# Kernel optimization log

Hardware: AMD Instinct MI355X
Metric: run time of the kernel (lower is better)

Reference implementation:

```python
import jax, jax.numpy as jnp
import numpy as np

# Mamba-2 config (from MambaBackbone defaults)
D_MODEL = 512
D_STATE = 64
D_CONV = 4
EXPAND = 2
HEADDIM = 64
CHUNK = 256
D_INNER = EXPAND * D_MODEL            # 1024
NHEADS = D_INNER // HEADDIM           # 16
CONV_DIM = D_INNER + 2 * D_STATE      # 1152 (ngroups=1)
D_IN_PROJ = 2 * D_INNER + 2 * D_STATE + NHEADS  # 2192


def setup_inputs() -> dict:
    key = jax.random.key(0)
    ks = jax.random.split(key, 8)
    B, T = 4, 4096
    x = jax.random.normal(ks[0], (B, T, D_MODEL), dtype=jnp.float32)
    W_in = jax.random.normal(ks[1], (D_IN_PROJ, D_MODEL), dtype=jnp.float32) * 0.02
    conv_w = jax.random.normal(ks[2], (CONV_DIM, D_CONV), dtype=jnp.float32) * 0.2
    conv_b = jnp.zeros((CONV_DIM,), jnp.float32)
    # dt_bias initialized so softplus(dt_bias) ~ Uniform-log[1e-3, 1e-1] (mamba2 init)
    dt0 = jnp.exp(jax.random.uniform(ks[3], (NHEADS,)) * (np.log(0.1) - np.log(0.001)) + np.log(0.001))
    dt_bias = dt0 + jnp.log(-jnp.expm1(-dt0))
    A_log = jnp.log(jnp.arange(1, NHEADS + 1, dtype=jnp.float32))  # A = -exp(A_log) in [-16,-1]
    D = jnp.ones((NHEADS,), jnp.float32)
    norm_w = jnp.ones((D_INNER,), jnp.float32)
    W_out = jax.random.normal(ks[4], (D_MODEL, D_INNER), dtype=jnp.float32) * 0.02
    return dict(x=x, W_in=W_in, conv_w=conv_w, conv_b=conv_b, dt_bias=dt_bias,
                A_log=A_log, D=D, norm_w=norm_w, W_out=W_out)


def segsum(a):
    """a: (..., l) -> (..., l, l) with [i,j] = sum_{j<k<=i} a[..,k]; -inf above diag."""
    l = a.shape[-1]
    cs = jnp.cumsum(a, axis=-1)
    ss = cs[..., :, None] - cs[..., None, :]
    mask = jnp.tril(jnp.ones((l, l), dtype=bool))
    return jnp.where(mask, ss, -jnp.inf)


def reference(x, W_in, conv_w, conv_b, dt_bias, A_log, D, norm_w, W_out):
    Bb, T, _ = x.shape
    # input projection -> [z | xBC | dt]
    zxbcdt = x @ W_in.T                                    # (B,T,2192)
    z = zxbcdt[..., :D_INNER]
    xBC = zxbcdt[..., D_INNER:D_INNER + CONV_DIM]
    dt = zxbcdt[..., -NHEADS:]
    # causal depthwise conv1d (kernel D_CONV) + SiLU
    xp = jnp.pad(xBC, ((0, 0), (D_CONV - 1, 0), (0, 0)))
    conv = sum(xp[:, k:k + T, :] * conv_w[:, k] for k in range(D_CONV)) + conv_b
    xBC = jax.nn.silu(conv)
    xs = xBC[..., :D_INNER].reshape(Bb, T, NHEADS, HEADDIM)  # (B,T,H,P)
    Bm = xBC[..., D_INNER:D_INNER + D_STATE]                 # (B,T,N)  ngroups=1
    Cm = xBC[..., D_INNER + D_STATE:]                        # (B,T,N)
    dt = jax.nn.softplus(dt + dt_bias)                       # (B,T,H)
    A = -jnp.exp(A_log)                                      # (H,)
    # ---- chunked SSD (Mamba-2) ----
    nc = T // CHUNK
    Ad = (dt * A).reshape(Bb, nc, CHUNK, NHEADS).transpose(0, 3, 1, 2)   # (b,h,c,l) log-decay
    x_dt = (xs * dt[..., None]).reshape(Bb, nc, CHUNK, NHEADS, HEADDIM)  # (b,c,l,h,p)
    Bc = Bm.reshape(Bb, nc, CHUNK, D_STATE)                              # (b,c,l,n)
    Cc = Cm.reshape(Bb, nc, CHUNK, D_STATE)
    A_cs = jnp.cumsum(Ad, axis=-1)                                       # (b,h,c,l)
    L = jnp.exp(segsum(Ad))                                              # (b,h,c,l,l)
    # intra-chunk (diagonal blocks)
    Y_diag = jnp.einsum('bcln,bcsn,bhcls,bcshp->bclhp', Cc, Bc, L, x_dt)
    # per-chunk end states
    decay_states = jnp.exp(A_cs[..., -1:] - A_cs)                        # (b,h,c,l)
    states = jnp.einsum('bcln,bhcl,bclhp->cbhpn', Bc, decay_states, x_dt)
    chunk_decay = jnp.exp(A_cs[..., -1]).transpose(2, 0, 1)              # (c,b,h)
    def step(h, inp):
        dec, st = inp
        return dec[..., None, None] * h + st, h                          # emit state BEFORE chunk
    h0 = jnp.zeros_like(states[0])
    _, prev = jax.lax.scan(step, h0, (chunk_decay, states))              # (c,b,h,p,n)
    # inter-chunk contribution
    Y_off = jnp.einsum('bcln,cbhpn,bhcl->bclhp', Cc, prev, jnp.exp(A_cs))
    y = (Y_diag + Y_off).reshape(Bb, T, NHEADS, HEADDIM) + D[None, None, :, None] * xs
    y = y.reshape(Bb, T, D_INNER)
    # gated RMSNorm: rmsnorm(y * silu(z)) * w   (norm_before_gate=False)
    yz = y * jax.nn.silu(z)
    out = yz * jax.lax.rsqrt(jnp.mean(yz * yz, axis=-1, keepdims=True) + 1e-5) * norm_w
    return out @ W_out.T
```

## Files before the change

### kernel.cpp

```cpp
#include <hip/hip_runtime.h>
#include <hip/hip_bf16.h>
#include <cstdint>

typedef unsigned int  uint;
typedef unsigned short ushort;
using bf16 = __hip_bfloat16;

#define B_     4
#define T_     4096
#define DM     512
#define DI     1024
#define DSTATE 64
#define HD     64
#define NH     16
#define NC     16
#define CHK    256
#define CONVD  1152
#define DPROJ  2192

using f32x4 = __attribute__((ext_vector_type(4))) float;
using s16x8 = __attribute__((ext_vector_type(8))) short;

#define MFMA16(a, b, c) __builtin_amdgcn_mfma_f32_16x16x32_bf16((a), (b), (c), 0, 0, 0)

__device__ inline void unpack8(const uint4 v, float* f) {
  const uint w[4] = {v.x, v.y, v.z, v.w};
#pragma unroll
  for (int i = 0; i < 4; ++i) {
    f[2*i]   = __uint_as_float(w[i] << 16);
    f[2*i+1] = __uint_as_float(w[i] & 0xffff0000u);
  }
}
__device__ inline void unpack4(const uint2 v, float* f) {
  f[0] = __uint_as_float(v.x << 16); f[1] = __uint_as_float(v.x & 0xffff0000u);
  f[2] = __uint_as_float(v.y << 16); f[3] = __uint_as_float(v.y & 0xffff0000u);
}
__device__ inline ushort bfbits(float a) {
  bf16 h = __float2bfloat16(a);
  return *reinterpret_cast<ushort*>(&h);
}
__device__ inline uint pack2(float a, float b) {
  return (uint)bfbits(a) | ((uint)bfbits(b) << 16);
}
__device__ inline uint4 pack8(const float* f) {
  uint4 v;
  v.x = pack2(f[0], f[1]); v.y = pack2(f[2], f[3]);
  v.z = pack2(f[4], f[5]); v.w = pack2(f[6], f[7]);
  return v;
}

__device__ __forceinline__ void gl_lds16(const void* g, void* l) {
  __builtin_amdgcn_global_load_lds(
      (const __attribute__((address_space(1))) unsigned int*)g,
      (__attribute__((address_space(3))) unsigned int*)l, 16, 0, 0);
}

__global__ __launch_bounds__(256)
void cast_bf16(const float* __restrict__ in, short* __restrict__ out, int n8) {
  const int i = blockIdx.x * 256 + threadIdx.x;
  if (i >= n8) return;
  float f[8];
  float4 a = *reinterpret_cast<const float4*>(&in[(size_t)i * 8]);
  float4 b = *reinterpret_cast<const float4*>(&in[(size_t)i * 8 + 4]);
  f[0]=a.x; f[1]=a.y; f[2]=a.z; f[3]=a.w; f[4]=b.x; f[5]=b.y; f[6]=b.z; f[7]=b.w;
  *reinterpret_cast<uint4*>(&out[(size_t)i * 8]) = pack8(f);
}

template<int EPI>
__global__ __launch_bounds__(256)
void gemm_mfma(const short* __restrict__ A, const short* __restrict__ Bw,
               int K, int N, int nbx, float* __restrict__ Cout,
               short* __restrict__ z, short* __restrict__ xbc,
               float* __restrict__ dtp, const float* __restrict__ dt_bias) {
  __shared__ __align__(16) char smem[(EPI == 1) ? 34816 : 32768];
  short* As = reinterpret_cast<short*>(smem);
  short* Bs = As + 128 * 64;
  const int tid  = threadIdx.x;
  const int lane = tid & 63, w = tid >> 6;
  const int hi = lane >> 4, lo = lane & 15;
  const int lx = lo & 7;
  const int wr = w >> 1, wc = w & 1;

  const int cpx = gridDim.x >> 3;
  const int swz = (blockIdx.x & 7) * cpx + (blockIdx.x >> 3);
  const int bm = (swz / nbx) * 128, bn = (swz % nbx) * 128;

  f32x4 acc[4][4] = {};

  const int srow = lane >> 3;
  const int scol = ((lane & 7) ^ srow) * 8;

  for (int k0 = 0; k0 < K; k0 += 64) {
#pragma unroll
    for (int i = 0; i < 4; ++i) {
      const int seg = w * 4 + i;
      const int row = seg * 8 + srow;
      gl_lds16(&A[(size_t)(bm + row) * K + k0 + scol], &As[seg * 512]);
      const int brow = (bn + row < N) ? (bn + row) : (N - 1);
      gl_lds16(&Bw[(size_t)brow * K + k0 + scol], &Bs[seg * 512]);
    }
    __syncthreads();
#pragma unroll
    for (int kb = 0; kb < 2; ++kb) {
      s16x8 af[4], bf[4];
#pragma unroll
      for (int t = 0; t < 4; ++t) {
        const int gg = ((kb * 4 + hi) ^ lx) * 8;
        af[t] = *reinterpret_cast<const s16x8*>(&As[(wr*64 + t*16 + lo) * 64 + gg]);
        bf[t] = *reinterpret_cast<const s16x8*>(&Bs[(wc*64 + t*16 + lo) * 64 + gg]);
      }
#pragma unroll
      for (int lt = 0; lt < 4; ++lt)
#pragma unroll
        for (int nt = 0; nt < 4; ++nt)
          acc[lt][nt] = MFMA16(af[lt], bf[nt], acc[lt][nt]);
    }
    __syncthreads();
  }

  if (EPI == 0) {
#pragma unroll
    for (int lt = 0; lt < 4; ++lt)
#pragma unroll
      for (int nt = 0; nt < 4; ++nt) {
        const int cg = bn + wc * 64 + nt * 16 + lo;
#pragma unroll
        for (int r = 0; r < 4; ++r) {
          const int rg = bm + wr * 64 + lt * 16 + hi * 4 + r;
          Cout[(size_t)rg * DM + cg] = acc[lt][nt][r];
        }
      }
  } else {
    if (bn + 128 > DI + CONVD) {
#pragma unroll
      for (int lt = 0; lt < 4; ++lt)
#pragma unroll
        for (int nt = 0; nt < 4; ++nt) {
          const int cg = bn + wc * 64 + nt * 16 + lo;
          if (cg >= DI + CONVD && cg < DPROJ) {
            const float bia = dt_bias[cg - DI - CONVD];
#pragma unroll
            for (int r = 0; r < 4; ++r) {
              const int rg = bm + wr * 64 + lt * 16 + hi * 4 + r;
              const float v = acc[lt][nt][r] + bia;
              dtp[(size_t)rg * NH + (cg - DI - CONVD)] =
                  (v > 20.f) ? v : log1pf(expf(v));
            }
          }
        }
    }
    ushort (*tile)[136] = reinterpret_cast<ushort(*)[136]>(smem);
    __syncthreads();
#pragma unroll
    for (int lt = 0; lt < 4; ++lt)
#pragma unroll
      for (int nt = 0; nt < 4; ++nt) {
        const int cl = wc * 64 + nt * 16 + lo;
#pragma unroll
        for (int r = 0; r < 4; ++r)
          tile[wr * 64 + lt * 16 + hi * 4 + r][cl] = bfbits(acc[lt][nt][r]);
      }
    __syncthreads();
#pragma unroll
    for (int it = 0; it < 8; ++it) {
      const int unit = it * 256 + tid;
      const int row = unit >> 4;
      const int c8  = (unit & 15) << 3;
      const int cg  = bn + c8;
      const int rg  = bm + row;
      if (cg >= DI + CONVD) continue;
      uint4 v = *reinterpret_cast<const uint4*>(&tile[row][c8]);
      if (cg < DI)
        *reinterpret_cast<uint4*>(&reinterpret_cast<ushort*>(z)[(size_t)rg * DI + cg]) = v;
      else
        *reinterpret_cast<uint4*>(&reinterpret_cast<ushort*>(xbc)[(size_t)rg * CONVD + (cg - DI)]) = v;
    }
  }
}

__global__ __launch_bounds__(256)
void conv_silu(const short* __restrict__ xbc, const float* __restrict__ cw,
               const float* __restrict__ cb, short* __restrict__ xc) {
  const int idx = blockIdx.x * 256 + threadIdx.x;
  const int cp = idx % 288;
  const int tb = idx / 288;
  const int ch = cp * 4;
  const int b  = tb >> 9;
  const int t0 = (tb & 511) << 3;
  const long base = ((long)b * T_ + t0) * CONVD + ch;

  float4 wv[4];
#pragma unroll
  for (int c = 0; c < 4; ++c)
    wv[c] = *reinterpret_cast<const float4*>(&cw[(ch + c) * 4]);
  const float4 bi = *reinterpret_cast<const float4*>(&cb[ch]);
  const float bias[4] = {bi.x, bi.y, bi.z, bi.w};

  float v[11][4];
#pragma unroll
  for (int i = 0; i < 11; ++i) {
    const int t = t0 - 3 + i;
    if (t >= 0) {
      const uint2 u = *reinterpret_cast<const uint2*>(&xbc[base + (long)(i - 3) * CONVD]);
      unpack4(u, v[i]);
    } else { v[i][0] = v[i][1] = v[i][2] = v[i][3] = 0.f; }
  }
#pragma unroll
  for (int j = 0; j < 8; ++j) {
    float s[4];
#pragma unroll
    for (int c = 0; c < 4; ++c) {
      s[c] = bias[c] + v[j][c]*wv[c].x + v[j+1][c]*wv[c].y
           + v[j+2][c]*wv[c].z + v[j+3][c]*wv[c].w;
      s[c] = s[c] / (1.f + __expf(-s[c]));
    }
    uint2 o; o.x = pack2(s[0], s[1]); o.y = pack2(s[2], s[3]);
    *reinterpret_cast<uint2*>(&xc[base + (long)j * CONVD]) = o;
  }
}

__global__ __launch_bounds__(256)
void ssd_states(const short* __restrict__ xc, const float* __restrict__ dtp,
                const float* __restrict__ A_log,
                float* __restrict__ acs_g, float* __restrict__ states) {
  const int bid = blockIdx.x;
  const int h = bid >> 6, b = (bid >> 4) & 3, c = bid & 15;
  const int tid = threadIdx.x;
  const int lane = tid & 63, w = tid >> 6;
  const int hi = lane >> 4, lo = lane & 15;

  __shared__ __align__(16) float acs[CHK];
  __shared__ float wsum[4];
  __shared__ __align__(16) uint Btm2[64 * 36];
  __shared__ __align__(16) uint Xdm2[64 * 36];

  const size_t row0 = (size_t)b * T_ + (size_t)c * CHK;

  const float Ah = -expf(A_log[h]);
  float v = dtp[(row0 + tid) * NH + h] * Ah;
#pragma unroll
  for (int off = 1; off < 64; off <<= 1) {
    const float u = __shfl_up(v, off);
    if (lane >= off) v += u;
  }
  if (lane == 63) wsum[w] = v;
  __syncthreads();
  float pre = 0.f;
#pragma unroll
  for (int ww = 0; ww < 4; ++ww) if (ww < w) pre += wsum[ww];
  v += pre;
  acs[tid] = v;
  acs_g[(((size_t)b * NH + h) * NC + c) * CHK + tid] = v;
  __syncthreads();
  const float acs_last = acs[CHK - 1];

  f32x4 stacc[4] = {};
  const int sp2 = tid & 31;
  const int g   = tid >> 5;

  for (int ss = 0; ss < 4; ++ss) {
    const int s0 = ss * 64;
    {
      const int se = s0 + 2 * sp2;
      const size_t re = (row0 + se) * (size_t)CONVD;
      const size_t ro = re + CONVD;
      uint4 bqe = *reinterpret_cast<const uint4*>(&xc[re + DI + g*8]);
      uint4 bqo = *reinterpret_cast<const uint4*>(&xc[ro + DI + g*8]);
      uint4 xqe = *reinterpret_cast<const uint4*>(&xc[re + h*HD + g*8]);
      uint4 xqo = *reinterpret_cast<const uint4*>(&xc[ro + h*HD + g*8]);
      const float de_ = dtp[(row0 + se) * NH + h] * __expf(acs_last - acs[se]);
      const float do_ = dtp[(row0 + se + 1) * NH + h] * __expf(acs_last - acs[se + 1]);
      const ushort* beu = reinterpret_cast<const ushort*>(&bqe);
      const ushort* bou = reinterpret_cast<const ushort*>(&bqo);
      float fe[8], fo[8];
      unpack8(xqe, fe); unpack8(xqo, fo);
#pragma unroll
      for (int j = 0; j < 8; ++j) {
        const int cidx = (g * 8 + j) * 36 + sp2;
        Btm2[cidx] = (uint)beu[j] | ((uint)bou[j] << 16);
        Xdm2[cidx] = pack2(fe[j] * de_, fo[j] * do_);
      }
    }
    __syncthreads();
#pragma unroll
    for (int kb = 0; kb < 2; ++kb) {
      s16x8 xdf = *reinterpret_cast<const s16x8*>(&Xdm2[(w*16 + lo)*36 + kb*16 + hi*4]);
#pragma unroll
      for (int nt = 0; nt < 4; ++nt) {
        s16x8 btf = *reinterpret_cast<const s16x8*>(&Btm2[(nt*16 + lo)*36 + kb*16 + hi*4]);
        stacc[nt] = MFMA16(xdf, btf, stacc[nt]);
      }
    }
    __syncthreads();
  }

  const size_t sbase = (((size_t)c * B_ + b) * NH + h) * (HD * DSTATE);
#pragma unroll
  for (int nt = 0; nt < 4; ++nt) {
    const int n = nt*16 + lo;
#pragma unroll
    for (int r = 0; r < 4; ++r) {
      const int p = w*16 + hi*4 + r;
      states[sbase + (size_t)p * DSTATE + n] = stacc[nt][r];
    }
  }
}

__global__ __launch_bounds__(256)
void chunk_scan(const float* __restrict__ acs_g, const float* __restrict__ st,
                short* __restrict__ pv) {
  const int idx = blockIdx.x * 256 + threadIdx.x;
  const int pn = idx & 4095;
  const int h  = (idx >> 12) & 15;
  const int b  = idx >> 16;
  float hst = 0.f;
#pragma unroll
  for (int c = 0; c < NC; ++c) {
    const size_t o = (((size_t)c * B_ + b) * NH + h) * 4096 + pn;
    reinterpret_cast<ushort*>(pv)[o] = bfbits(hst);
    const float dec = __expf(acs_g[(((size_t)b * NH + h) * NC + c) * CHK + CHK - 1]);
    hst = dec * hst + st[o];
  }
}

__global__ __launch_bounds__(256, 2)
void ssd_y(const short* __restrict__ xc, const float* __restrict__ dtp,
           const float* __restrict__ acs_g, const short* __restrict__ pv,
           const float* __restrict__ Dvec, short* __restrict__ y) {
  const int bid = blockIdx.x;
  const int h = bid >> 6, b = (bid >> 4) & 3, c = bid & 15;
  const int tid = threadIdx.x;
  const int lane = tid & 63, w = tid >> 6;
  const int hi = lane >> 4, lo = lane & 15;

  __shared__ __align__(16) float acs[CHK];
  __shared__ __align__(16) float ds[CHK];
  __shared__ __align__(16) short Bsm[64 * 64];
  __shared__ __align__(16) uint Xtm2[64 * 36];
  __shared__ __align__(16) short Pb[4][16][72];

  const size_t row0 = (size_t)b * T_ + (size_t)c * CHK;
  const float* acg = &acs_g[(((size_t)b * NH + h) * NC + c) * CHK];

  acs[tid] = acg[tid];
  __syncthreads();
  ds[tid] = (tid > 0) ? __expf(acs[tid] - acs[tid - 1]) : 1.f;

  s16x8 creg[4][2];
#pragma unroll
  for (int lt = 0; lt < 4; ++lt)
#pragma unroll
    for (int kb = 0; kb < 2; ++kb)
      creg[lt][kb] = *reinterpret_cast<const s16x8*>(
          &xc[(row0 + w*64 + lt*16 + lo) * CONVD + DI + DSTATE + kb*32 + hi*8]);

  f32x4 yacc[4][4] = {};
  {
    const short* pvb = &pv[(((size_t)c * B_ + b) * NH + h) * 4096];
    __builtin_amdgcn_s_setprio(1);
#pragma unroll
    for (int kb = 0; kb < 2; ++kb) {
      s16x8 pf[4];
#pragma unroll
      for (int pt = 0; pt < 4; ++pt)
        pf[pt] = *reinterpret_cast<const s16x8*>(&pvb[(pt*16 + lo) * DSTATE + kb*32 + hi*8]);
#pragma unroll
      for (int pt = 0; pt < 4; ++pt)
#pragma unroll
        for (int lt = 0; lt < 4; ++lt)
          yacc[pt][lt] = MFMA16(pf[pt], creg[lt][kb], yacc[pt][lt]);
    }
    __builtin_amdgcn_s_setprio(0);
  }
  __syncthreads();
#pragma unroll
  for (int lt = 0; lt < 4; ++lt) {
    const float el = __expf(acs[w*64 + lt*16 + lo]);
#pragma unroll
    for (int pt = 0; pt < 4; ++pt)
#pragma unroll
      for (int r = 0; r < 4; ++r) yacc[pt][lt][r] *= el;
  }

  const int sp2 = tid & 31;
  const int g   = tid >> 5;
  const int srow8 = lane >> 3;
  const int gsrc  = ((lane & 7) ^ srow8) * 8;

  for (int ss = 0; ss < 4; ++ss) {
    const int s0 = ss * 64;
#pragma unroll
    for (int i = 0; i < 2; ++i) {
      const int seg = w * 2 + i;
      gl_lds16(&xc[(row0 + s0 + seg * 8 + srow8) * (size_t)CONVD + DI + gsrc],
               &Bsm[seg * 512]);
    }
    {
      const int se = s0 + 2 * sp2;
      const size_t re = (row0 + se) * (size_t)CONVD;
      uint4 xqe = *reinterpret_cast<const uint4*>(&xc[re + h*HD + g*8]);
      uint4 xqo = *reinterpret_cast<const uint4*>(&xc[re + CONVD + h*HD + g*8]);
      const float de_ = dtp[(row0 + se) * NH + h];
      const float do_ = dtp[(row0 + se + 1) * NH + h];
      float fe[8], fo[8];
      unpack8(xqe, fe); unpack8(xqo, fo);
#pragma unroll
      for (int j = 0; j < 8; ++j)
        Xtm2[(g * 8 + j) * 36 + sp2] = pack2(fe[j] * de_, fo[j] * do_);
    }
    __syncthreads();

    if (ss <= w) {
#pragma unroll
      for (int lt = 0; lt < 4; ++lt) {
        f32x4 sacc[4] = {};
        __builtin_amdgcn_s_setprio(1);
#pragma unroll
        for (int st = 0; st < 4; ++st) {
          const int r = st * 16 + lo;
          s16x8 b0 = *reinterpret_cast<const s16x8*>(&Bsm[r*64 + ((0*4 + hi) ^ (lo & 7)) * 8]);
          s16x8 b1 = *reinterpret_cast<const s16x8*>(&Bsm[r*64 + ((1*4 + hi) ^ (lo & 7)) * 8]);
          sacc[st] = MFMA16(b0, creg[lt][0], sacc[st]);
          sacc[st] = MFMA16(b1, creg[lt][1], sacc[st]);
        }
        __builtin_amdgcn_s_setprio(0);
        const int lg = w*64 + lt*16 + lo;
        const float al = acs[lg];
#pragma unroll
        for (int st = 0; st < 4; ++st) {
          const int sb = s0 + st*16 + hi*4;
          float wv[4];
          wv[3] = __expf(al - acs[sb + 3]);
          wv[2] = wv[3] * ds[sb + 3];
          wv[1] = wv[2] * ds[sb + 2];
          wv[0] = wv[1] * ds[sb + 1];
          float p4[4];
#pragma unroll
          for (int r = 0; r < 4; ++r)
            p4[r] = (sb + r <= lg) ? sacc[st][r] * wv[r] : 0.f;
          uint2 pk; pk.x = pack2(p4[0], p4[1]); pk.y = pack2(p4[2], p4[3]);
          *reinterpret_cast<uint2*>(&Pb[w][lo][st*16 + hi*4]) = pk;
        }
        __builtin_amdgcn_s_setprio(1);
#pragma unroll
        for (int kb = 0; kb < 2; ++kb) {
          s16x8 pfr = *reinterpret_cast<const s16x8*>(&Pb[w][lo][kb*32 + hi*8]);
#pragma unroll
          for (int pt = 0; pt < 4; ++pt) {
            s16x8 xfr = *reinterpret_cast<const s16x8*>(&Xtm2[(pt*16 + lo)*36 + kb*16 + hi*4]);
            yacc[pt][lt] = MFMA16(xfr, pfr, yacc[pt][lt]);
          }
        }
        __builtin_amdgcn_s_setprio(0);
      }
    }
    __syncthreads();
  }

  const float Dh = Dvec[h];
#pragma unroll
  for (int lt = 0; lt < 4; ++lt) {
    const int l = w*64 + lt*16 + lo;
    ushort* yrow = reinterpret_cast<ushort*>(&y[(row0 + l) * DI + h * HD]);
    const short* xrow = &xc[(row0 + l) * CONVD + h * HD];
#pragma unroll
    for (int pt = 0; pt < 4; ++pt) {
      const int p0 = pt*16 + hi*4;
      uint2 xb2 = *reinterpret_cast<const uint2*>(&xrow[p0]);
      float xf[4]; unpack4(xb2, xf);
      float o[4];
#pragma unroll
      for (int r = 0; r < 4; ++r) o[r] = yacc[pt][lt][r] + Dh * xf[r];
      uint2 pk; pk.x = pack2(o[0], o[1]); pk.y = pack2(o[2], o[3]);
      *reinterpret_cast<uint2*>(&yrow[p0]) = pk;
    }
  }
}

__global__ __launch_bounds__(256)
void gate_rmsnorm(const short* __restrict__ z, const float* __restrict__ norm_w,
                  short* __restrict__ y) {
  const int row = blockIdx.x;
  const int tid = threadIdx.x;
  const short* zrow = &z[(size_t)row * DI];
  short* yrow = &y[(size_t)row * DI];
  uint2 yb = *reinterpret_cast<const uint2*>(&yrow[tid * 4]);
  uint2 zb = *reinterpret_cast<const uint2*>(&zrow[tid * 4]);
  float yv[4], zv[4];
  unpack4(yb, yv); unpack4(zb, zv);
  float tq[4];
  float ss = 0.f;
#pragma unroll
  for (int j = 0; j < 4; ++j) {
    const float sil = zv[j] / (1.f + __expf(-zv[j]));
    tq[j] = yv[j] * sil;
    ss += tq[j] * tq[j];
  }
#pragma unroll
  for (int off = 32; off >= 1; off >>= 1) ss += __shfl_down(ss, off);
  __shared__ float red[4];
  if ((tid & 63) == 0) red[tid >> 6] = ss;
  __syncthreads();
  const float tot = red[0] + red[1] + red[2] + red[3];
  const float r = rsqrtf(tot * (1.f / (float)DI) + 1e-5f);
  float4 wv = *reinterpret_cast<const float4*>(&norm_w[tid * 4]);
  uint2 ob;
  ob.x = pack2(tq[0] * r * wv.x, tq[1] * r * wv.y);
  ob.y = pack2(tq[2] * r * wv.z, tq[3] * r * wv.w);
  *reinterpret_cast<uint2*>(&yrow[tid * 4]) = ob;
}

extern "C" void kernel_launch(void* const* d_in, const int* in_sizes, int n_in,
                              void* d_out, int out_size, void* d_ws, size_t ws_size,
                              hipStream_t stream) {
  const float* x       = (const float*)d_in[0];
  const float* W_in    = (const float*)d_in[1];
  const float* conv_w  = (const float*)d_in[2];
  const float* conv_b  = (const float*)d_in[3];
  const float* dt_bias = (const float*)d_in[4];
  const float* A_log   = (const float*)d_in[5];
  const float* Dv      = (const float*)d_in[6];
  const float* norm_w  = (const float*)d_in[7];
  const float* W_out   = (const float*)d_in[8];
  float* out = (float*)d_out;

  char* w0 = (char*)d_ws;
  short* z    = (short*)(w0);
  short* xbc  = (short*)(w0 + 33554432ULL);
  short* xc   = (short*)(w0 + 71303168ULL);
  short* wob  = (short*)(w0 + 109051904ULL);
  float* dtp  = (float*)(w0 + 111149056ULL);
  float* acs  = (float*)(w0 + 112197632ULL);
  float* st   = (float*)(w0 + 113246208ULL);
  short* pv   = (short*)(w0 + 130023424ULL);
  short* xb   = xc;
  short* wb   = (short*)st;
  short* y    = xbc;

  const int M = B_ * T_;

  cast_bf16<<<(M * DM / 8 + 255) / 256, 256, 0, stream>>>(x, xb, M * DM / 8);
  cast_bf16<<<(DPROJ * DM / 8 + 255) / 256, 256, 0, stream>>>(W_in, wb, DPROJ * DM / 8);
  cast_bf16<<<(DM * DI / 8 + 255) / 256, 256, 0, stream>>>(W_out, wob, DM * DI / 8);

  const int nbx_in = (DPROJ + 127) / 128;
  gemm_mfma<1><<<nbx_in * (M / 128), 256, 0, stream>>>(
      xb, wb, DM, DPROJ, nbx_in, nullptr, z, xbc, dtp, dt_bias);
  conv_silu<<<(M / 8) * 288 / 256, 256, 0, stream>>>(xbc, conv_w, conv_b, xc);
  ssd_states<<<B_ * NC * NH, 256, 0, stream>>>(xc, dtp, A_log, acs, st);
  chunk_scan<<<(B_ * NH * HD * DSTATE) / 256, 256, 0, stream>>>(acs, st, pv);
  ssd_y<<<B_ * NC * NH, 256, 0, stream>>>(xc, dtp, acs, pv, Dv, y);
  gate_rmsnorm<<<M, 256, 0, stream>>>(z, norm_w, y);
  gemm_mfma<0><<<(DM / 128) * (M / 128), 256, 0, stream>>>(
      y, wob, DI, DM, DM / 128, out, nullptr, nullptr, nullptr, nullptr);
}
```

Baseline: 208.6 us.

## Split-K output GEMM with atomics and preload whole chunk in ssd_y

The output projection GEMM becomes a split-K kernel over two K halves that accumulates into a zeroed output buffer with float atomics, doubling the grid from 512 to 1024 blocks to raise occupancy. ssd_y now loads all 256 rows of B and the dt-scaled X^T for the chunk into LDS once up front, removing the per-subchunk barriers and loads from the intra-chunk loop. The costs are a memset, atomic write traffic and non-deterministic summation order, plus much larger LDS use in ssd_y (about 67KB) that may cut occupancy below its two-blocks launch bound.

```diff
diff --git a/kernel.cpp b/kernel.cpp
--- a/kernel.cpp
+++ b/kernel.cpp
@@ -66,13 +66,12 @@
   *reinterpret_cast<uint4*>(&out[(size_t)i * 8]) = pack8(f);
 }
 
-template<int EPI>
 __global__ __launch_bounds__(256)
-void gemm_mfma(const short* __restrict__ A, const short* __restrict__ Bw,
-               int K, int N, int nbx, float* __restrict__ Cout,
-               short* __restrict__ z, short* __restrict__ xbc,
-               float* __restrict__ dtp, const float* __restrict__ dt_bias) {
-  __shared__ __align__(16) char smem[(EPI == 1) ? 34816 : 32768];
+void gemm_in_mfma(const short* __restrict__ A, const short* __restrict__ Bw,
+                  short* __restrict__ z, short* __restrict__ xbc,
+                  float* __restrict__ dtp, const float* __restrict__ dt_bias) {
+  const int K = DM, N = DPROJ, nbx = 18;
+  __shared__ __align__(16) char smem[34816];
   short* As = reinterpret_cast<short*>(smem);
   short* Bs = As + 128 * 64;
   const int tid  = threadIdx.x;
@@ -118,64 +117,113 @@
     __syncthreads();
   }
 
-  if (EPI == 0) {
+  if (bn + 128 > DI + CONVD) {
 #pragma unroll
     for (int lt = 0; lt < 4; ++lt)
 #pragma unroll
       for (int nt = 0; nt < 4; ++nt) {
         const int cg = bn + wc * 64 + nt * 16 + lo;
-#pragma unroll
-        for (int r = 0; r < 4; ++r) {
-          const int rg = bm + wr * 64 + lt * 16 + hi * 4 + r;
-          Cout[(size_t)rg * DM + cg] = acc[lt][nt][r];
-        }
-      }
-  } else {
-    if (bn + 128 > DI + CONVD) {
-#pragma unroll
-      for (int lt = 0; lt < 4; ++lt)
-#pragma unroll
-        for (int nt = 0; nt < 4; ++nt) {
-          const int cg = bn + wc * 64 + nt * 16 + lo;
-          if (cg >= DI + CONVD && cg < DPROJ) {
-            const float bia = dt_bias[cg - DI - CONVD];
-#pragma unroll
-            for (int r = 0; r < 4; ++r) {
-              const int rg = bm + wr * 64 + lt * 16 + hi * 4 + r;
-              const float v = acc[lt][nt][r] + bia;
-              dtp[(size_t)rg * NH + (cg - DI - CONVD)] =
-                  (v > 20.f) ? v : log1pf(expf(v));
-            }
+        if (cg >= DI + CONVD && cg < DPROJ) {
+          const float bia = dt_bias[cg - DI - CONVD];
+#pragma unroll
+          for (int r = 0; r < 4; ++r) {
+            const int rg = bm + wr * 64 + lt * 16 + hi * 4 + r;
+            const float v = acc[lt][nt][r] + bia;
+            dtp[(size_t)rg * NH + (cg - DI - CONVD)] =
+                (v > 20.f) ? v : log1pf(expf(v));
           }
         }
-    }
-    ushort (*tile)[136] = reinterpret_cast<ushort(*)[136]>(smem);
+      }
+  }
+  ushort (*tile)[136] = reinterpret_cast<ushort(*)[136]>(smem);
+  __syncthreads();
+#pragma unroll
+  for (int lt = 0; lt < 4; ++lt)
+#pragma unroll
+    for (int nt = 0; nt < 4; ++nt) {
+      const int cl = wc * 64 + nt * 16 + lo;
+#pragma unroll
+      for (int r = 0; r < 4; ++r)
+        tile[wr * 64 + lt * 16 + hi * 4 + r][cl] = bfbits(acc[lt][nt][r]);
+    }
+  __syncthreads();
+#pragma unroll
+  for (int it = 0; it < 8; ++it) {
+    const int unit = it * 256 + tid;
+    const int row = unit >> 4;
+    const int c8  = (unit & 15) << 3;
+    const int cg  = bn + c8;
+    const int rg  = bm + row;
+    if (cg >= DI + CONVD) continue;
+    uint4 v = *reinterpret_cast<const uint4*>(&tile[row][c8]);
+    if (cg < DI)
+      *reinterpret_cast<uint4*>(&reinterpret_cast<ushort*>(z)[(size_t)rg * DI + cg]) = v;
+    else
+      *reinterpret_cast<uint4*>(&reinterpret_cast<ushort*>(xbc)[(size_t)rg * CONVD + (cg - DI)]) = v;
+  }
+}
+
+__global__ __launch_bounds__(256)
+void gemm_out_mfma(const short* __restrict__ A, const short* __restrict__ Bw,
+                   float* __restrict__ C) {
+  const int K = DI;
+  __shared__ __align__(16) short As[128 * 64];
+  __shared__ __align__(16) short Bs[128 * 64];
+  const int tid  = threadIdx.x;
+  const int lane = tid & 63, w = tid >> 6;
+  const int hi = lane >> 4, lo = lane & 15;
+  const int lx = lo & 7;
+  const int wr = w >> 1, wc = w & 1;
+
+  const int cpx = gridDim.x >> 3;
+  const int swz = (blockIdx.x & 7) * cpx + (blockIdx.x >> 3);
+  const int m = swz >> 3, n = (swz >> 1) & 3, kh = swz & 1;
+  const int bm = m * 128, bn = n * 128;
+  const int kbase = kh * (K / 2);
+
+  f32x4 acc[4][4] = {};
+
+  const int srow = lane >> 3;
+  const int scol = ((lane & 7) ^ srow) * 8;
+
+  for (int k0 = kbase; k0 < kbase + K / 2; k0 += 64) {
+#pragma unroll
+    for (int i = 0; i < 4; ++i) {
+      const int seg = w * 4 + i;
+      const int row = seg * 8 + srow;
+      gl_lds16(&A[(size_t)(bm + row) * K + k0 + scol], &As[seg * 512]);
+      gl_lds16(&Bw[(size_t)(bn + row) * K + k0 + scol], &Bs[seg * 512]);
+    }
     __syncthreads();
 #pragma unroll
-    for (int lt = 0; lt < 4; ++lt)
-#pragma unroll
-      for (int nt = 0; nt < 4; ++nt) {
-        const int cl = wc * 64 + nt * 16 + lo;
-#pragma unroll
-        for (int r = 0; r < 4; ++r)
-          tile[wr * 64 + lt * 16 + hi * 4 + r][cl] = bfbits(acc[lt][nt][r]);
-      }
+    for (int kb = 0; kb < 2; ++kb) {
+      s16x8 af[4], bf[4];
+#pragma unroll
+      for (int t = 0; t < 4; ++t) {
+        const int gg = ((kb * 4 + hi) ^ lx) * 8;
+        af[t] = *reinterpret_cast<const s16x8*>(&As[(wr*64 + t*16 + lo) * 64 + gg]);
+        bf[t] = *reinterpret_cast<const s16x8*>(&Bs[(wc*64 + t*16 + lo) * 64 + gg]);
+      }
+#pragma unroll
+      for (int lt = 0; lt < 4; ++lt)
+#pragma unroll
+        for (int nt = 0; nt < 4; ++nt)
+          acc[lt][nt] = MFMA16(af[lt], bf[nt], acc[lt][nt]);
+    }
     __syncthreads();
-#pragma unroll
-    for (int it = 0; it < 8; ++it) {
-      const int unit = it * 256 + tid;
-      const int row = unit >> 4;
-      const int c8  = (unit & 15) << 3;
-      const int cg  = bn + c8;
-      const int rg  = bm + row;
-      if (cg >= DI + CONVD) continue;
-      uint4 v = *reinterpret_cast<const uint4*>(&tile[row][c8]);
-      if (cg < DI)
-        *reinterpret_cast<uint4*>(&reinterpret_cast<ushort*>(z)[(size_t)rg * DI + cg]) = v;
-      else
-        *reinterpret_cast<uint4*>(&reinterpret_cast<ushort*>(xbc)[(size_t)rg * CONVD + (cg - DI)]) = v;
-    }
-  }
+  }
+
+#pragma unroll
+  for (int lt = 0; lt < 4; ++lt)
+#pragma unroll
+    for (int nt = 0; nt < 4; ++nt) {
+      const int cg = bn + wc * 64 + nt * 16 + lo;
+#pragma unroll
+      for (int r = 0; r < 4; ++r) {
+        const int rg = bm + wr * 64 + lt * 16 + hi * 4 + r;
+        unsafeAtomicAdd(&C[(size_t)rg * DM + cg], acc[lt][nt][r]);
+      }
+    }
 }
 
 __global__ __launch_bounds__(256)
@@ -335,8 +383,8 @@
 
   __shared__ __align__(16) float acs[CHK];
   __shared__ __align__(16) float ds[CHK];
-  __shared__ __align__(16) short Bsm[64 * 64];
-  __shared__ __align__(16) uint Xtm2[64 * 36];
+  __shared__ __align__(16) short Bsm[256 * 64];
+  __shared__ __align__(16) uint Xtm2[64 * 132];
   __shared__ __align__(16) short Pb[4][16][72];
 
   const size_t row0 = (size_t)b * T_ + (size_t)c * CHK;
@@ -345,6 +393,31 @@
   acs[tid] = acg[tid];
   __syncthreads();
   ds[tid] = (tid > 0) ? __expf(acs[tid] - acs[tid - 1]) : 1.f;
+
+  const int srow8 = lane >> 3;
+  const int gsrc  = ((lane & 7) ^ srow8) * 8;
+#pragma unroll
+  for (int i = 0; i < 8; ++i) {
+    const int seg = w * 8 + i;
+    gl_lds16(&xc[(row0 + seg * 8 + srow8) * (size_t)CONVD + DI + gsrc],
+             &Bsm[seg * 512]);
+  }
+  const int sp2 = tid & 31;
+  const int g   = tid >> 5;
+#pragma unroll
+  for (int ss = 0; ss < 4; ++ss) {
+    const int se = ss * 64 + 2 * sp2;
+    const size_t re = (row0 + se) * (size_t)CONVD;
+    uint4 xqe = *reinterpret_cast<const uint4*>(&xc[re + h*HD + g*8]);
+    uint4 xqo = *reinterpret_cast<const uint4*>(&xc[re + CONVD + h*HD + g*8]);
+    const float de_ = dtp[(row0 + se) * NH + h];
+    const float do_ = dtp[(row0 + se + 1) * NH + h];
+    float fe[8], fo[8];
+    unpack8(xqe, fe); unpack8(xqo, fo);
+#pragma unroll
+    for (int j = 0; j < 8; ++j)
+      Xtm2[(g * 8 + j) * 132 + ss * 32 + sp2] = pack2(fe[j] * de_, fo[j] * do_);
+  }
 
   s16x8 creg[4][2];
 #pragma unroll
@@ -372,7 +445,6 @@
     }
     __builtin_amdgcn_s_setprio(0);
   }
-  __syncthreads();
 #pragma unroll
   for (int lt = 0; lt < 4; ++lt) {
     const float el = __expf(acs[w*64 + lt*16 + lo]);
@@ -381,80 +453,54 @@
 #pragma unroll
       for (int r = 0; r < 4; ++r) yacc[pt][lt][r] *= el;
   }
-
-  const int sp2 = tid & 31;
-  const int g   = tid >> 5;
-  const int srow8 = lane >> 3;
-  const int gsrc  = ((lane & 7) ^ srow8) * 8;
-
-  for (int ss = 0; ss < 4; ++ss) {
+  __syncthreads();
+
+  const int lxx = lo & 7;
+  for (int ss = 0; ss <= w; ++ss) {
     const int s0 = ss * 64;
 #pragma unroll
-    for (int i = 0; i < 2; ++i) {
-      const int seg = w * 2 + i;
-      gl_lds16(&xc[(row0 + s0 + seg * 8 + srow8) * (size_t)CONVD + DI + gsrc],
-               &Bsm[seg * 512]);
-    }
-    {
-      const int se = s0 + 2 * sp2;
-      const size_t re = (row0 + se) * (size_t)CONVD;
-      uint4 xqe = *reinterpret_cast<const uint4*>(&xc[re + h*HD + g*8]);
-      uint4 xqo = *reinterpret_cast<const uint4*>(&xc[re + CONVD + h*HD + g*8]);
-      const float de_ = dtp[(row0 + se) * NH + h];
-      const float do_ = dtp[(row0 + se + 1) * NH + h];
-      float fe[8], fo[8];
-      unpack8(xqe, fe); unpack8(xqo, fo);
-#pragma unroll
-      for (int j = 0; j < 8; ++j)
-        Xtm2[(g * 8 + j) * 36 + sp2] = pack2(fe[j] * de_, fo[j] * do_);
-    }
-    __syncthreads();
-
-    if (ss <= w) {
-#pragma unroll
-      for (int lt = 0; lt < 4; ++lt) {
-        f32x4 sacc[4] = {};
-        __builtin_amdgcn_s_setprio(1);
-#pragma unroll
-        for (int st = 0; st < 4; ++st) {
-          const int r = st * 16 + lo;
-          s16x8 b0 = *reinterpret_cast<const s16x8*>(&Bsm[r*64 + ((0*4 + hi) ^ (lo & 7)) * 8]);
-          s16x8 b1 = *reinterpret_cast<const s16x8*>(&Bsm[r*64 + ((1*4 + hi) ^ (lo & 7)) * 8]);
-          sacc[st] = MFMA16(b0, creg[lt][0], sacc[st]);
-          sacc[st] = MFMA16(b1, creg[lt][1], sacc[st]);
+    for (int lt = 0; lt < 4; ++lt) {
+      f32x4 sacc[4] = {};
+      __builtin_amdgcn_s_setprio(1);
+#pragma unroll
+      for (int st = 0; st < 4; ++st) {
+        const int r = s0 + st * 16 + lo;
+        s16x8 b0 = *reinterpret_cast<const s16x8*>(&Bsm[r*64 + ((0*4 + hi) ^ lxx) * 8]);
+        s16x8 b1 = *reinterpret_cast<const s16x8*>(&Bsm[r*64 + ((1*4 + hi) ^ lxx) * 8]);
+        sacc[st] = MFMA16(b0, creg[lt][0], sacc[st]);
+        sacc[st] = MFMA16(b1, creg[lt][1], sacc[st]);
+      }
+      __builtin_amdgcn_s_setprio(0);
+      const int lg = w*64 + lt*16 + lo;
+      const float al = acs[lg];
+#pragma unroll
+      for (int st = 0; st < 4; ++st) {
+        const int sb = s0 + st*16 + hi*4;
+        float wv[4];
+        wv[3] = __expf(al - acs[sb + 3]);
+        wv[2] = wv[3] * ds[sb + 3];
+        wv[1] = wv[2] * ds[sb + 2];
+        wv[0] = wv[1] * ds[sb + 1];
+        float p4[4];
+#pragma unroll
+        for (int r = 0; r < 4; ++r)
+          p4[r] = (sb + r <= lg) ? sacc[st][r] * wv[r] : 0.f;
+        uint2 pk; pk.x = pack2(p4[0], p4[1]); pk.y = pack2(p4[2], p4[3]);
+        *reinterpret_cast<uint2*>(&Pb[w][lo][st*16 + hi*4]) = pk;
+      }
+      __builtin_amdgcn_s_setprio(1);
+#pragma unroll
+      for (int kb = 0; kb < 2; ++kb) {
+        s16x8 pfr = *reinterpret_cast<const s16x8*>(&Pb[w][lo][kb*32 + hi*8]);
+#pragma unroll
+        for (int pt = 0; pt < 4; ++pt) {
+          s16x8 xfr = *reinterpret_cast<const s16x8*>(
+              &Xtm2[(pt*16 + lo)*132 + ss*32 + kb*16 + hi*4]);
+          yacc[pt][lt] = MFMA16(xfr, pfr, yacc[pt][lt]);
         }
-        __builtin_amdgcn_s_setprio(0);
-        const int lg = w*64 + lt*16 + lo;
-        const float al = acs[lg];
-#pragma unroll
-        for (int st = 0; st < 4; ++st) {
-          const int sb = s0 + st*16 + hi*4;
-          float wv[4];
-          wv[3] = __expf(al - acs[sb + 3]);
-          wv[2] = wv[3] * ds[sb + 3];
-          wv[1] = wv[2] * ds[sb + 2];
-          wv[0] = wv[1] * ds[sb + 1];
-          float p4[4];
-#pragma unroll
-          for (int r = 0; r < 4; ++r)
-            p4[r] = (sb + r <= lg) ? sacc[st][r] * wv[r] : 0.f;
-          uint2 pk; pk.x = pack2(p4[0], p4[1]); pk.y = pack2(p4[2], p4[3]);
-          *reinterpret_cast<uint2*>(&Pb[w][lo][st*16 + hi*4]) = pk;
-        }
-        __builtin_amdgcn_s_setprio(1);
-#pragma unroll
-        for (int kb = 0; kb < 2; ++kb) {
-          s16x8 pfr = *reinterpret_cast<const s16x8*>(&Pb[w][lo][kb*32 + hi*8]);
-#pragma unroll
-          for (int pt = 0; pt < 4; ++pt) {
-            s16x8 xfr = *reinterpret_cast<const s16x8*>(&Xtm2[(pt*16 + lo)*36 + kb*16 + hi*4]);
-            yacc[pt][lt] = MFMA16(xfr, pfr, yacc[pt][lt]);
-          }
-        }
-        __builtin_amdgcn_s_setprio(0);
-      }
-    }
-    __syncthreads();
+      }
+      __builtin_amdgcn_s_setprio(0);
+    }
   }
 
   const float Dh = Dvec[h];
@@ -539,18 +585,17 @@
 
   const int M = B_ * T_;
 
+  hipMemsetAsync(out, 0, (size_t)M * DM * sizeof(float), stream);
+
   cast_bf16<<<(M * DM / 8 + 255) / 256, 256, 0, stream>>>(x, xb, M * DM / 8);
   cast_bf16<<<(DPROJ * DM / 8 + 255) / 256, 256, 0, stream>>>(W_in, wb, DPROJ * DM / 8);
   cast_bf16<<<(DM * DI / 8 + 255) / 256, 256, 0, stream>>>(W_out, wob, DM * DI / 8);
 
-  const int nbx_in = (DPROJ + 127) / 128;
-  gemm_mfma<1><<<nbx_in * (M / 128), 256, 0, stream>>>(
-      xb, wb, DM, DPROJ, nbx_in, nullptr, z, xbc, dtp, dt_bias);
+  gemm_in_mfma<<<18 * (M / 128), 256, 0, stream>>>(xb, wb, z, xbc, dtp, dt_bias);
   conv_silu<<<(M / 8) * 288 / 256, 256, 0, stream>>>(xbc, conv_w, conv_b, xc);
   ssd_states<<<B_ * NC * NH, 256, 0, stream>>>(xc, dtp, A_log, acs, st);
   chunk_scan<<<(B_ * NH * HD * DSTATE) / 256, 256, 0, stream>>>(acs, st, pv);
   ssd_y<<<B_ * NC * NH, 256, 0, stream>>>(xc, dtp, acs, pv, Dv, y);
   gate_rmsnorm<<<M, 256, 0, stream>>>(z, norm_w, y);
-  gemm_mfma<0><<<(DM / 128) * (M / 128), 256, 0, stream>>>(
-      y, wob, DI, DM, DM / 128, out, nullptr, nullptr, nullptr, nullptr);
-}
+  gemm_out_mfma<<<2 * (DM / 128) * (M / 128), 256, 0, stream>>>(y, wob, out);
+}
```

Result: slower. 253.6 us (+21.5%).
